# Kernel tuning notes

Hardware: AMD Instinct MI355X
Metric: run time of the kernel (lower is better)

Reference implementation:

```python
import jax, jax.numpy as jnp
import numpy as np

N_NODES = 100000

def sage_conv(x, edge_index, Wl, bl, Wr):
    # PyG SAGEConv, aggr='add', normalize=False:
    #   out = lin_l(sum_{j in N(i)} x_j) + lin_r(x_i)
    src, dst = edge_index[0], edge_index[1]
    agg = jax.ops.segment_sum(x[src], dst, num_segments=N_NODES)  # [N, F]
    return agg @ Wl.T + bl + x @ Wr.T


def setup_inputs() -> dict:
    key = jax.random.key(0)
    ks = jax.random.split(key, 7)
    F_IN, HID, C, E = 128, 256, 50, 640000
    x = jax.random.normal(ks[0], (N_NODES, F_IN), dtype=jnp.float32)
    edge_index = jax.random.randint(ks[1], (2, E), 0, N_NODES, dtype=jnp.int64)
    s1 = 1.0 / np.sqrt(F_IN)
    s2 = 1.0 / np.sqrt(HID)
    return {
        "x": x,
        "edge_index": edge_index,
        "W1l": jax.random.normal(ks[2], (HID, F_IN), dtype=jnp.float32) * s1,
        "b1l": jnp.zeros((HID,), dtype=jnp.float32),
        "W1r": jax.random.normal(ks[3], (HID, F_IN), dtype=jnp.float32) * s1,
        "W2l": jax.random.normal(ks[4], (C, HID), dtype=jnp.float32) * s2,
        "b2l": jnp.zeros((C,), dtype=jnp.float32),
        "W2r": jax.random.normal(ks[5], (C, HID), dtype=jnp.float32) * s2,
    }


def reference(x, edge_index, W1l, b1l, W1r, W2l, b2l, W2r):
    h = sage_conv(x, edge_index, W1l, b1l, W1r)
    h = jax.nn.relu(h)
    # F.dropout(p=0.5, training=False) is identity in eval mode
    out = sage_conv(h, edge_index, W2l, b2l, W2r)
    return out
```

## Files before the change

### kernel.cpp

```cpp
#include <hip/hip_runtime.h>

#define N_NODES 100000
#define MPAD    100096
#define F_IN 128
#define HID 256
#define C_OUT 50
#define N_EDGES 640000
#define CAP 32
#define NXCD 8
#define NODES_PER_XCD 12500
#define NSLICES 256
#define EPS (N_EDGES / NSLICES)

typedef __attribute__((ext_vector_type(8))) short short8;
typedef __attribute__((ext_vector_type(8))) ushort us8;
typedef __attribute__((ext_vector_type(4))) float f32x4;

struct alignas(8) us4 { ushort x, y, z, w; };

__device__ __forceinline__ ushort f2bf(float f) {
    union { float f; unsigned u; } v; v.f = f;
    unsigned r = (v.u + 0x7fffu + ((v.u >> 16) & 1u)) >> 16;
    return (ushort)r;
}

__device__ __forceinline__ float bf2f(ushort u) {
    union { unsigned u; float f; } v; v.u = ((unsigned)u) << 16;
    return v.f;
}

__device__ __forceinline__ void load_lds16(const void* gsrc, void* lds) {
    __builtin_amdgcn_global_load_lds(
        (const __attribute__((address_space(1))) void*)gsrc,
        (__attribute__((address_space(3))) void*)lds, 16, 0, 0);
}

__global__ void prep_kernel(const float* __restrict__ W1l, const float* __restrict__ W1r,
                            const float* __restrict__ W2l, const float* __restrict__ W2r,
                            ushort* __restrict__ B1t, ushort* __restrict__ B2t,
                            int* __restrict__ cnt) {
    int idx = blockIdx.x * blockDim.x + threadIdx.x;
    if (idx < N_NODES) cnt[idx] = 0;
    if (idx < 256 * 256) {
        int o = idx >> 8, k = idx & 255;
        float v = (k < 128) ? W1l[o * 128 + k] : W1r[o * 128 + (k - 128)];
        B1t[o * 256 + k] = f2bf(v);
    }
    if (idx < 128 * 256) {
        int c = idx >> 8, k = idx & 255;
        float v = 0.f;
        if (c < C_OUT) v = W2l[c * 256 + k];
        else if (c >= 64 && c < 64 + C_OUT) v = W2r[(c - 64) * 256 + k];
        B2t[c * 256 + k] = f2bf(v);
    }
}

__global__ __launch_bounds__(256) void scatter_xcd(const int* __restrict__ src,
                                                   const int* __restrict__ dst,
                                                   int* __restrict__ cnt,
                                                   int* __restrict__ bucket) {
    int xcd = blockIdx.x & (NXCD - 1);
    int slice = blockIdx.x >> 3;
    int lo = xcd * NODES_PER_XCD;
    int hi = lo + NODES_PER_XCD;
    int base = slice * EPS;
    for (int i = base + threadIdx.x; i < base + EPS; i += 256) {
        int d = dst[i];
        int s = src[i];
        if (d >= lo && d < hi) {
            int p = atomicAdd(&cnt[d], 1);
            if (p < CAP) bucket[(size_t)d * CAP + p] = s;
        }
    }
}

__global__ void xcvt_kernel(const float* __restrict__ x, ushort* __restrict__ A1) {
    int tid = blockIdx.x * blockDim.x + threadIdx.x;
    int node = tid >> 5, q = tid & 31;
    if (node >= N_NODES) return;
    float4 v = *reinterpret_cast<const float4*>(x + (size_t)node * F_IN + q * 4);
    us4 o;
    o.x = f2bf(v.x); o.y = f2bf(v.y); o.z = f2bf(v.z); o.w = f2bf(v.w);
    *reinterpret_cast<us4*>(&A1[(size_t)node * 256 + 128 + q * 4]) = o;
}

__global__ void gather1_kernel(const int* __restrict__ cnt, const int* __restrict__ bucket,
                               ushort* __restrict__ A1) {
    int tid = blockIdx.x * blockDim.x + threadIdx.x;
    int node = tid >> 4, q = tid & 15;
    if (node >= N_NODES) return;
    int n = cnt[node];
    if (n > CAP) n = CAP;
    const int* row = bucket + (size_t)node * CAP;
    float a[8];
#pragma unroll
    for (int j = 0; j < 8; ++j) a[j] = 0.f;
    int p = 0;
    for (; p + 4 <= n; p += 4) {
        int s0 = row[p], s1 = row[p + 1], s2 = row[p + 2], s3 = row[p + 3];
        us8 v0 = *reinterpret_cast<const us8*>(&A1[(size_t)s0 * 256 + 128 + q * 8]);
        us8 v1 = *reinterpret_cast<const us8*>(&A1[(size_t)s1 * 256 + 128 + q * 8]);
        us8 v2 = *reinterpret_cast<const us8*>(&A1[(size_t)s2 * 256 + 128 + q * 8]);
        us8 v3 = *reinterpret_cast<const us8*>(&A1[(size_t)s3 * 256 + 128 + q * 8]);
#pragma unroll
        for (int j = 0; j < 8; ++j) a[j] += bf2f(v0[j]);
#pragma unroll
        for (int j = 0; j < 8; ++j) a[j] += bf2f(v1[j]);
#pragma unroll
        for (int j = 0; j < 8; ++j) a[j] += bf2f(v2[j]);
#pragma unroll
        for (int j = 0; j < 8; ++j) a[j] += bf2f(v3[j]);
    }
    int rem = n - p;
    if (rem > 0) {
        int s0 = row[p];
        int s1 = (rem > 1) ? row[p + 1] : s0;
        int s2 = (rem > 2) ? row[p + 2] : s0;
        us8 v0 = *reinterpret_cast<const us8*>(&A1[(size_t)s0 * 256 + 128 + q * 8]);
        us8 v1 = *reinterpret_cast<const us8*>(&A1[(size_t)s1 * 256 + 128 + q * 8]);
        us8 v2 = *reinterpret_cast<const us8*>(&A1[(size_t)s2 * 256 + 128 + q * 8]);
#pragma unroll
        for (int j = 0; j < 8; ++j) a[j] += bf2f(v0[j]);
        if (rem > 1) {
#pragma unroll
            for (int j = 0; j < 8; ++j) a[j] += bf2f(v1[j]);
        }
        if (rem > 2) {
#pragma unroll
            for (int j = 0; j < 8; ++j) a[j] += bf2f(v2[j]);
        }
    }
    us8 o;
#pragma unroll
    for (int j = 0; j < 8; ++j) o[j] = f2bf(a[j]);
    *reinterpret_cast<us8*>(&A1[(size_t)node * 256 + q * 8]) = o;
}

__global__ void gather2_kernel(const ushort* __restrict__ g, const int* __restrict__ cnt,
                               const int* __restrict__ bucket, float* __restrict__ out) {
    int tid = blockIdx.x * blockDim.x + threadIdx.x;
    int node = tid >> 3, q = tid & 7;
    if (node >= N_NODES) return;
    int c = q * 8;
    if (c >= C_OUT) return;
    int n = cnt[node];
    if (n > CAP) n = CAP;
    const int* row = bucket + (size_t)node * CAP;
    float a[8];
#pragma unroll
    for (int j = 0; j < 8; ++j) a[j] = 0.f;
    int p = 0;
    for (; p + 4 <= n; p += 4) {
        int s0 = row[p], s1 = row[p + 1], s2 = row[p + 2], s3 = row[p + 3];
        us8 v0 = *reinterpret_cast<const us8*>(&g[(size_t)s0 * 64 + c]);
        us8 v1 = *reinterpret_cast<const us8*>(&g[(size_t)s1 * 64 + c]);
        us8 v2 = *reinterpret_cast<const us8*>(&g[(size_t)s2 * 64 + c]);
        us8 v3 = *reinterpret_cast<const us8*>(&g[(size_t)s3 * 64 + c]);
#pragma unroll
        for (int j = 0; j < 8; ++j) a[j] += bf2f(v0[j]);
#pragma unroll
        for (int j = 0; j < 8; ++j) a[j] += bf2f(v1[j]);
#pragma unroll
        for (int j = 0; j < 8; ++j) a[j] += bf2f(v2[j]);
#pragma unroll
        for (int j = 0; j < 8; ++j) a[j] += bf2f(v3[j]);
    }
    int rem = n - p;
    if (rem > 0) {
        int s0 = row[p];
        int s1 = (rem > 1) ? row[p + 1] : s0;
        int s2 = (rem > 2) ? row[p + 2] : s0;
        us8 v0 = *reinterpret_cast<const us8*>(&g[(size_t)s0 * 64 + c]);
        us8 v1 = *reinterpret_cast<const us8*>(&g[(size_t)s1 * 64 + c]);
        us8 v2 = *reinterpret_cast<const us8*>(&g[(size_t)s2 * 64 + c]);
#pragma unroll
        for (int j = 0; j < 8; ++j) a[j] += bf2f(v0[j]);
        if (rem > 1) {
#pragma unroll
            for (int j = 0; j < 8; ++j) a[j] += bf2f(v1[j]);
        }
        if (rem > 2) {
#pragma unroll
            for (int j = 0; j < 8; ++j) a[j] += bf2f(v2[j]);
        }
    }
    float* po = out + (size_t)node * C_OUT;
#pragma unroll
    for (int j = 0; j < 8; ++j) {
        if (c + j < C_OUT) po[c + j] += a[j];
    }
}

template <int EPI>
__global__ __launch_bounds__(256) void mfma_gemm(
    const ushort* __restrict__ A, const ushort* __restrict__ B,
    const float* __restrict__ bias, ushort* __restrict__ hOut,
    ushort* __restrict__ gOut, float* __restrict__ oOut) {
    __shared__ alignas(16) ushort As[128 * 32];
    __shared__ alignas(16) ushort Bs[128 * 32];
    const int tid = threadIdx.x;
    const int lane = tid & 63, wid = tid >> 6;
    const int wr = wid >> 1, wc = wid & 1;
    const int brow = blockIdx.x, bcol = blockIdx.y;

    f32x4 acc[4][4];
#pragma unroll
    for (int m = 0; m < 4; ++m)
#pragma unroll
        for (int n = 0; n < 4; ++n) acc[m][n] = (f32x4){0.f, 0.f, 0.f, 0.f};

    const int c0 = tid, c1 = tid + 256;
    const int r0 = c0 >> 2, k80 = (c0 & 3) * 8;
    const int r1 = c1 >> 2, k81 = (c1 & 3) * 8;
    const size_t aRow0 = (size_t)(brow * 128 + r0) * 256;
    const size_t aRow1 = (size_t)(brow * 128 + r1) * 256;
    const size_t bRow0 = (size_t)(bcol * 128 + r0) * 256;
    const size_t bRow1 = (size_t)(bcol * 128 + r1) * 256;

    const int aoffA = (lane & 15) * 32 + (lane >> 4) * 8;

    for (int kt = 0; kt < 8; ++kt) {
        const int kOff = kt * 32;
        load_lds16(A + aRow0 + kOff + k80, &As[c0 * 8]);
        load_lds16(A + aRow1 + kOff + k81, &As[c1 * 8]);
        load_lds16(B + bRow0 + kOff + k80, &Bs[c0 * 8]);
        load_lds16(B + bRow1 + kOff + k81, &Bs[c1 * 8]);
        __syncthreads();

        short8 af[4], bfr[4];
#pragma unroll
        for (int m = 0; m < 4; ++m)
            af[m] = *reinterpret_cast<const short8*>(&As[(wr * 64 + m * 16) * 32 + aoffA]);
#pragma unroll
        for (int n = 0; n < 4; ++n)
            bfr[n] = *reinterpret_cast<const short8*>(&Bs[(wc * 64 + n * 16) * 32 + aoffA]);
#pragma unroll
        for (int m = 0; m < 4; ++m)
#pragma unroll
            for (int n = 0; n < 4; ++n)
                acc[m][n] = __builtin_amdgcn_mfma_f32_16x16x32_bf16(af[m], bfr[n], acc[m][n], 0, 0, 0);
        __syncthreads();
    }

    const int colB = bcol * 128 + wc * 64 + (lane & 15);
    const int rowB = brow * 128 + wr * 64 + ((lane >> 4) << 2);

    if (EPI == 1) {
        float bv[4];
#pragma unroll
        for (int n = 0; n < 4; ++n) bv[n] = bias[colB + n * 16];
#pragma unroll
        for (int m = 0; m < 4; ++m) {
#pragma unroll
            for (int r = 0; r < 4; ++r) {
                int row = rowB + m * 16 + r;
                if (row >= N_NODES) continue;
#pragma unroll
                for (int n = 0; n < 4; ++n) {
                    float v = acc[m][n][r] + bv[n];
                    v = v > 0.f ? v : 0.f;
                    hOut[(size_t)row * 256 + colB + n * 16] = f2bf(v);
                }
            }
        }
    } else {
#pragma unroll
        for (int m = 0; m < 4; ++m) {
#pragma unroll
            for (int r = 0; r < 4; ++r) {
                int row = rowB + m * 16 + r;
                if (row >= N_NODES) continue;
#pragma unroll
                for (int n = 0; n < 4; ++n) {
                    int cg = colB + n * 16;
                    float v = acc[m][n][r];
                    if (cg < 64) {
                        gOut[(size_t)row * 64 + cg] = f2bf(v);
                    } else if (cg < 64 + C_OUT) {
                        oOut[(size_t)row * C_OUT + (cg - 64)] = v + bias[cg - 64];
                    }
                }
            }
        }
    }
}

extern "C" void kernel_launch(void* const* d_in, const int* in_sizes, int n_in,
                              void* d_out, int out_size, void* d_ws, size_t ws_size,
                              hipStream_t stream) {
    const float* x   = (const float*)d_in[0];
    const int*   ei  = (const int*)d_in[1];
    const float* W1l = (const float*)d_in[2];
    const float* b1l = (const float*)d_in[3];
    const float* W1r = (const float*)d_in[4];
    const float* W2l = (const float*)d_in[5];
    const float* b2l = (const float*)d_in[6];
    const float* W2r = (const float*)d_in[7];
    float* out = (float*)d_out;

    ushort* A1   = (ushort*)d_ws;
    ushort* hbuf = A1 + (size_t)MPAD * 256;
    ushort* B1t  = hbuf + (size_t)MPAD * 256;
    ushort* B2t  = B1t + 256 * 256;
    ushort* g    = B2t + 128 * 256;
    int* cnt     = (int*)(g + (size_t)N_NODES * 64);
    int* bucket  = cnt + N_NODES;

    const int* src = ei;
    const int* dst = ei + N_EDGES;

    prep_kernel<<<391, 256, 0, stream>>>(W1l, W1r, W2l, W2r, B1t, B2t, cnt);
    scatter_xcd<<<NSLICES * NXCD, 256, 0, stream>>>(src, dst, cnt, bucket);

    xcvt_kernel<<<(N_NODES * 32 + 255) / 256, 256, 0, stream>>>(x, A1);
    gather1_kernel<<<(N_NODES * 16 + 255) / 256, 256, 0, stream>>>(cnt, bucket, A1);

    const int nbrow = MPAD / 128;
    mfma_gemm<1><<<dim3(nbrow, 2), 256, 0, stream>>>(A1, B1t, b1l, hbuf, nullptr, nullptr);
    mfma_gemm<2><<<dim3(nbrow, 1), 256, 0, stream>>>(hbuf, B2t, b2l, nullptr, g, out);

    gather2_kernel<<<(N_NODES * 8 + 255) / 256, 256, 0, stream>>>(g, cnt, bucket, out);
}
```

Measured before the change: 167.1 us.

## Use hardware XCC id with atomic work-stealing in scatter; deepen gather unroll to 8

The scatter kernel now reads the real XCC id from a hardware register and pulls edge slices from per-partition atomic cursors. Each block works its own XCD's node range first, then steals slices from the other ranges, so destination-node atomics stay local to one XCD's L2 instead of relying on the assumed round-robin block-to-XCD mapping. Both gather kernels now issue 8 neighbor loads per iteration instead of 4, and the remainder path handles up to 7 in one batch, to raise memory-level parallelism. The tradeoff is extra cursor atomics, two __syncthreads per slice, and more registers in the gathers.

```diff
diff --git a/kernel.cpp b/kernel.cpp
--- a/kernel.cpp
+++ b/kernel.cpp
@@ -38,9 +38,10 @@
 __global__ void prep_kernel(const float* __restrict__ W1l, const float* __restrict__ W1r,
                             const float* __restrict__ W2l, const float* __restrict__ W2r,
                             ushort* __restrict__ B1t, ushort* __restrict__ B2t,
-                            int* __restrict__ cnt) {
+                            int* __restrict__ cnt, int* __restrict__ cursors) {
     int idx = blockIdx.x * blockDim.x + threadIdx.x;
     if (idx < N_NODES) cnt[idx] = 0;
+    if (idx < NXCD) cursors[idx] = 0;
     if (idx < 256 * 256) {
         int o = idx >> 8, k = idx & 255;
         float v = (k < 128) ? W1l[o * 128 + k] : W1r[o * 128 + (k - 128)];
@@ -55,21 +56,33 @@
     }
 }
 
-__global__ __launch_bounds__(256) void scatter_xcd(const int* __restrict__ src,
-                                                   const int* __restrict__ dst,
-                                                   int* __restrict__ cnt,
-                                                   int* __restrict__ bucket) {
-    int xcd = blockIdx.x & (NXCD - 1);
-    int slice = blockIdx.x >> 3;
-    int lo = xcd * NODES_PER_XCD;
-    int hi = lo + NODES_PER_XCD;
-    int base = slice * EPS;
-    for (int i = base + threadIdx.x; i < base + EPS; i += 256) {
-        int d = dst[i];
-        int s = src[i];
-        if (d >= lo && d < hi) {
-            int p = atomicAdd(&cnt[d], 1);
-            if (p < CAP) bucket[(size_t)d * CAP + p] = s;
+__global__ __launch_bounds__(256) void scatter_xcd2(const int* __restrict__ src,
+                                                    const int* __restrict__ dst,
+                                                    int* __restrict__ cnt,
+                                                    int* __restrict__ bucket,
+                                                    int* __restrict__ cursors) {
+    unsigned myxcd;
+    asm volatile("s_getreg_b32 %0, hwreg(HW_REG_XCC_ID)" : "=s"(myxcd));
+    myxcd &= (NXCD - 1);
+    __shared__ int s_slice;
+    for (int k = 0; k < NXCD; ++k) {
+        int q = (myxcd + k) & (NXCD - 1);
+        int lo = q * NODES_PER_XCD;
+        int hi = lo + NODES_PER_XCD;
+        while (true) {
+            if (threadIdx.x == 0) s_slice = atomicAdd(&cursors[q], 1);
+            __syncthreads();
+            int slice = s_slice;
+            __syncthreads();
+            if (slice >= NSLICES) break;
+            int base = slice * EPS;
+            for (int i = base + (int)threadIdx.x; i < base + EPS; i += 256) {
+                int d = dst[i];
+                if (d >= lo && d < hi) {
+                    int p = atomicAdd(&cnt[d], 1);
+                    if (p < CAP) bucket[(size_t)d * CAP + p] = src[i];
+                }
+            }
         }
     }
 }
@@ -96,38 +109,33 @@
 #pragma unroll
     for (int j = 0; j < 8; ++j) a[j] = 0.f;
     int p = 0;
-    for (; p + 4 <= n; p += 4) {
-        int s0 = row[p], s1 = row[p + 1], s2 = row[p + 2], s3 = row[p + 3];
-        us8 v0 = *reinterpret_cast<const us8*>(&A1[(size_t)s0 * 256 + 128 + q * 8]);
-        us8 v1 = *reinterpret_cast<const us8*>(&A1[(size_t)s1 * 256 + 128 + q * 8]);
-        us8 v2 = *reinterpret_cast<const us8*>(&A1[(size_t)s2 * 256 + 128 + q * 8]);
-        us8 v3 = *reinterpret_cast<const us8*>(&A1[(size_t)s3 * 256 + 128 + q * 8]);
-#pragma unroll
-        for (int j = 0; j < 8; ++j) a[j] += bf2f(v0[j]);
-#pragma unroll
-        for (int j = 0; j < 8; ++j) a[j] += bf2f(v1[j]);
-#pragma unroll
-        for (int j = 0; j < 8; ++j) a[j] += bf2f(v2[j]);
-#pragma unroll
-        for (int j = 0; j < 8; ++j) a[j] += bf2f(v3[j]);
+    while (p + 8 <= n) {
+        us8 v[8];
+#pragma unroll
+        for (int t = 0; t < 8; ++t) {
+            int s = row[p + t];
+            v[t] = *reinterpret_cast<const us8*>(&A1[(size_t)s * 256 + 128 + q * 8]);
+        }
+#pragma unroll
+        for (int t = 0; t < 8; ++t)
+#pragma unroll
+            for (int j = 0; j < 8; ++j) a[j] += bf2f(v[t][j]);
+        p += 8;
     }
     int rem = n - p;
     if (rem > 0) {
-        int s0 = row[p];
-        int s1 = (rem > 1) ? row[p + 1] : s0;
-        int s2 = (rem > 2) ? row[p + 2] : s0;
-        us8 v0 = *reinterpret_cast<const us8*>(&A1[(size_t)s0 * 256 + 128 + q * 8]);
-        us8 v1 = *reinterpret_cast<const us8*>(&A1[(size_t)s1 * 256 + 128 + q * 8]);
-        us8 v2 = *reinterpret_cast<const us8*>(&A1[(size_t)s2 * 256 + 128 + q * 8]);
-#pragma unroll
-        for (int j = 0; j < 8; ++j) a[j] += bf2f(v0[j]);
-        if (rem > 1) {
-#pragma unroll
-            for (int j = 0; j < 8; ++j) a[j] += bf2f(v1[j]);
-        }
-        if (rem > 2) {
-#pragma unroll
-            for (int j = 0; j < 8; ++j) a[j] += bf2f(v2[j]);
+        us8 v[7];
+#pragma unroll
+        for (int t = 0; t < 7; ++t) {
+            int s = (t < rem) ? row[p + t] : row[p];
+            v[t] = *reinterpret_cast<const us8*>(&A1[(size_t)s * 256 + 128 + q * 8]);
+        }
+#pragma unroll
+        for (int t = 0; t < 7; ++t) {
+            if (t < rem) {
+#pragma unroll
+                for (int j = 0; j < 8; ++j) a[j] += bf2f(v[t][j]);
+            }
         }
     }
     us8 o;
@@ -150,38 +158,33 @@
 #pragma unroll
     for (int j = 0; j < 8; ++j) a[j] = 0.f;
     int p = 0;
-    for (; p + 4 <= n; p += 4) {
-        int s0 = row[p], s1 = row[p + 1], s2 = row[p + 2], s3 = row[p + 3];
-        us8 v0 = *reinterpret_cast<const us8*>(&g[(size_t)s0 * 64 + c]);
-        us8 v1 = *reinterpret_cast<const us8*>(&g[(size_t)s1 * 64 + c]);
-        us8 v2 = *reinterpret_cast<const us8*>(&g[(size_t)s2 * 64 + c]);
-        us8 v3 = *reinterpret_cast<const us8*>(&g[(size_t)s3 * 64 + c]);
-#pragma unroll
-        for (int j = 0; j < 8; ++j) a[j] += bf2f(v0[j]);
-#pragma unroll
-        for (int j = 0; j < 8; ++j) a[j] += bf2f(v1[j]);
-#pragma unroll
-        for (int j = 0; j < 8; ++j) a[j] += bf2f(v2[j]);
-#pragma unroll
-        for (int j = 0; j < 8; ++j) a[j] += bf2f(v3[j]);
+    while (p + 8 <= n) {
+        us8 v[8];
+#pragma unroll
+        for (int t = 0; t < 8; ++t) {
+            int s = row[p + t];
+            v[t] = *reinterpret_cast<const us8*>(&g[(size_t)s * 64 + c]);
+        }
+#pragma unroll
+        for (int t = 0; t < 8; ++t)
+#pragma unroll
+            for (int j = 0; j < 8; ++j) a[j] += bf2f(v[t][j]);
+        p += 8;
     }
     int rem = n - p;
     if (rem > 0) {
-        int s0 = row[p];
-        int s1 = (rem > 1) ? row[p + 1] : s0;
-        int s2 = (rem > 2) ? row[p + 2] : s0;
-        us8 v0 = *reinterpret_cast<const us8*>(&g[(size_t)s0 * 64 + c]);
-        us8 v1 = *reinterpret_cast<const us8*>(&g[(size_t)s1 * 64 + c]);
-        us8 v2 = *reinterpret_cast<const us8*>(&g[(size_t)s2 * 64 + c]);
-#pragma unroll
-        for (int j = 0; j < 8; ++j) a[j] += bf2f(v0[j]);
-        if (rem > 1) {
-#pragma unroll
-            for (int j = 0; j < 8; ++j) a[j] += bf2f(v1[j]);
-        }
-        if (rem > 2) {
-#pragma unroll
-            for (int j = 0; j < 8; ++j) a[j] += bf2f(v2[j]);
+        us8 v[7];
+#pragma unroll
+        for (int t = 0; t < 7; ++t) {
+            int s = (t < rem) ? row[p + t] : row[p];
+            v[t] = *reinterpret_cast<const us8*>(&g[(size_t)s * 64 + c]);
+        }
+#pragma unroll
+        for (int t = 0; t < 7; ++t) {
+            if (t < rem) {
+#pragma unroll
+                for (int j = 0; j < 8; ++j) a[j] += bf2f(v[t][j]);
+            }
         }
     }
     float* po = out + (size_t)node * C_OUT;
@@ -304,13 +307,14 @@
     ushort* B2t  = B1t + 256 * 256;
     ushort* g    = B2t + 128 * 256;
     int* cnt     = (int*)(g + (size_t)N_NODES * 64);
-    int* bucket  = cnt + N_NODES;
+    int* cursors = cnt + N_NODES;
+    int* bucket  = cursors + 64;
 
     const int* src = ei;
     const int* dst = ei + N_EDGES;
 
-    prep_kernel<<<391, 256, 0, stream>>>(W1l, W1r, W2l, W2r, B1t, B2t, cnt);
-    scatter_xcd<<<NSLICES * NXCD, 256, 0, stream>>>(src, dst, cnt, bucket);
+    prep_kernel<<<391, 256, 0, stream>>>(W1l, W1r, W2l, W2r, B1t, B2t, cnt, cursors);
+    scatter_xcd2<<<2048, 256, 0, stream>>>(src, dst, cnt, bucket, cursors);
 
     xcvt_kernel<<<(N_NODES * 32 + 255) / 256, 256, 0, stream>>>(x, A1);
     gather1_kernel<<<(N_NODES * 16 + 255) / 256, 256, 0, stream>>>(cnt, bucket, A1);
```

Measured after the change: 371.1 us. 122% more time.
